# Optimization experiments

Measured on AMD Instinct MI355X. Metric: run time of the kernel, lower is better.

Reference implementation:

```python
import jax, jax.numpy as jnp
import numpy as np

N = 50000   # nodes
E = 500000  # edges
NEG_SLOPE = 0.2


def _edge_softmax(e, dst, n):
    # softmax over edges grouped by destination node (DGL edge_softmax)
    m = jax.ops.segment_max(e, dst, num_segments=n)          # [N,H]
    ex = jnp.exp(e - m[dst])
    s = jax.ops.segment_sum(ex, dst, num_segments=n)
    return ex / s[dst]


def _gat(h, W, al, ar, b, src, dst, heads, d, Wres=None, act=True):
    # DGL GATConv (eval mode, no dropout)
    n = h.shape[0]
    feat = (h @ W).reshape(n, heads, d)                      # [N,H,D]
    el = jnp.sum(feat * al[None], axis=-1)                   # [N,H]
    er = jnp.sum(feat * ar[None], axis=-1)                   # [N,H]
    e = jax.nn.leaky_relu(el[src] + er[dst], NEG_SLOPE)      # [E,H]
    a = _edge_softmax(e, dst, n)                             # [E,H]
    rst = jax.ops.segment_sum(feat[src] * a[..., None], dst, num_segments=n)  # [N,H,D]
    if Wres is not None:
        res = (h @ Wres).reshape(n, heads, d)
    else:
        res = h.reshape(n, heads, d)                         # identity residual (in == heads*d)
    rst = rst + res + b.reshape(1, heads, d)
    if act:
        rst = jax.nn.elu(rst)
    return rst.reshape(n, heads * d)


def _bn(x, g, b, m, v):
    # BatchNorm1d in eval mode
    return (x - m) * g * jax.lax.rsqrt(v + 1e-5) + b


def setup_inputs() -> dict:
    key = jax.random.key(0)
    ks = jax.random.split(key, 40)
    rn = lambda i, s: jax.random.normal(ks[i], s, jnp.float32) * 0.1
    inp = dict(
        node_feats=jax.random.normal(ks[0], (N, 128), jnp.float32),
        edge_feats=jax.random.normal(ks[1], (E, 64), jnp.float32),
        src=jax.random.randint(ks[2], (E,), 0, N, jnp.int32),
        dst=jax.random.randint(ks[3], (E,), 0, N, jnp.int32),
        # GAT layer 0: 128 -> 8 heads x 16
        W0=rn(4, (128, 128)), al0=rn(5, (8, 16)), ar0=rn(6, (8, 16)), b0=rn(7, (128,)),
        g0=1.0 + rn(8, (128,)), bt0=rn(9, (128,)), m0=rn(10, (128,)),
        v0=1.0 + 0.1 * jax.random.uniform(ks[11], (128,), jnp.float32),
        # GAT layer 1: 128 -> 8 heads x 8 (residual projection)
        W1=rn(12, (128, 64)), al1=rn(13, (8, 8)), ar1=rn(14, (8, 8)), b1=rn(15, (64,)),
        Wres1=rn(16, (128, 64)),
        g1=1.0 + rn(17, (64,)), bt1=rn(18, (64,)), m1=rn(19, (64,)),
        v1=1.0 + 0.1 * jax.random.uniform(ks[20], (64,), jnp.float32),
        # GAT layer 2: 64 -> 1 head x 32 (residual projection, no activation)
        W2=rn(21, (64, 32)), al2=rn(22, (1, 32)), ar2=rn(23, (1, 32)), b2=rn(24, (32,)),
        Wres2=rn(25, (64, 32)),
        g2=1.0 + rn(26, (32,)), bt2=rn(27, (32,)), m2=rn(28, (32,)),
        v2=1.0 + 0.1 * jax.random.uniform(ks[29], (32,), jnp.float32),
        # edge projection 64 -> 128
        We=rn(30, (64, 128)), be=rn(31, (128,)),
        # edge classifier: 192 -> 32 -> 16 -> 2
        Wc1=rn(32, (192, 32)), bc1=rn(33, (32,)),
        Wc2=rn(34, (32, 16)), bc2=rn(35, (16,)),
        Wc3=rn(36, (16, 2)), bc3=rn(37, (2,)),
    )
    return inp


def reference(node_feats, edge_feats, src, dst,
              W0, al0, ar0, b0, g0, bt0, m0, v0,
              W1, al1, ar1, b1, Wres1, g1, bt1, m1, v1,
              W2, al2, ar2, b2, Wres2, g2, bt2, m2, v2,
              We, be, Wc1, bc1, Wc2, bc2, Wc3, bc3):
    h = _bn(_gat(node_feats, W0, al0, ar0, b0, src, dst, 8, 16), g0, bt0, m0, v0)
    h = _bn(_gat(h, W1, al1, ar1, b1, src, dst, 8, 8, Wres1), g1, bt1, m1, v1)
    h = _bn(_gat(h, W2, al2, ar2, b2, src, dst, 1, 32, Wres2, act=False), g2, bt2, m2, v2)
    ef = jax.nn.relu(edge_feats @ We + be)                   # [E,128]
    rep = jnp.concatenate([h[src], h[dst], ef], axis=1)      # [E,192]
    z = jax.nn.relu(rep @ Wc1 + bc1)
    z = jax.nn.relu(z @ Wc2 + bc2)
    return z @ Wc3 + bc3                                     # [E,2]
```

## Files before the change

### kernel.cpp

```cpp
#include <hip/hip_runtime.h>
#include <cfloat>
#include <math.h>

#define NEG_SLOPE 0.2f

typedef short short8 __attribute__((ext_vector_type(8)));
typedef float f32x4 __attribute__((ext_vector_type(4)));

__device__ __forceinline__ short f2bf(float x) {
    unsigned u = __float_as_uint(x);
    u += 0x7fffu + ((u >> 16) & 1u);
    return (short)(u >> 16);
}

__device__ __forceinline__ void lds_fence() {
    __asm__ __volatile__("s_waitcnt lgkmcnt(0)" ::: "memory");
}


__global__ void count_deg_k(const int* __restrict__ dst, int* __restrict__ deg, int E) {
    int i = blockIdx.x * 256 + threadIdx.x;
    if (i < E) atomicAdd(&deg[dst[i]], 1);
}

__global__ void scan_k(const int* __restrict__ deg, int* __restrict__ off, int n) {
    __shared__ int part[1024];
    int tid = threadIdx.x;
    int chunk = (n + 1023) >> 10;
    int beg = tid * chunk;
    int end = min(beg + chunk, n);
    int s = 0;
    for (int i = beg; i < end; ++i) s += deg[i];
    part[tid] = s;
    __syncthreads();
    for (int d = 1; d < 1024; d <<= 1) {
        int v = (tid >= d) ? part[tid - d] : 0;
        __syncthreads();
        part[tid] += v;
        __syncthreads();
    }
    int run = (tid > 0) ? part[tid - 1] : 0;
    for (int i = beg; i < end; ++i) { off[i] = run; run += deg[i]; }
    if (tid == 1023) off[n] = part[1023];
}

__global__ void scatter_k(const int* __restrict__ src, const int* __restrict__ dst,
                          const int* __restrict__ off, int* __restrict__ cur,
                          int* __restrict__ srcp, int E) {
    int i = blockIdx.x * 256 + threadIdx.x;
    if (i >= E) return;
    int d = dst[i];
    int p = off[d] + atomicAdd(&cur[d], 1);
    srcp[p] = src[i];
}


__global__ void conv_w_k(const float* __restrict__ We, const float* __restrict__ Wc1p,
                         const float* __restrict__ Wc2,
                         short* __restrict__ WeTg, short* __restrict__ Wc1Tg,
                         short* __restrict__ Wc2Tg) {
    int t = blockIdx.x * 256 + threadIdx.x;
    if (t < 64 * 128) { int k = t >> 7, n = t & 127; WeTg[n * 64 + k] = f2bf(We[t]); }
    if (t < 128 * 32) { int k = t >> 5, n = t & 31; Wc1Tg[n * 128 + k] = f2bf(Wc1p[t]); }
    if (t < 32 * 16)  { int k = t >> 4, n = t & 15; Wc2Tg[n * 32 + k] = f2bf(Wc2[t]); }
}


template<int K, int OUT>
__global__ __launch_bounds__(256) void gemm2_k(const float* __restrict__ A,
                                               const float* __restrict__ B1, float* __restrict__ C1,
                                               const float* __restrict__ B2, float* __restrict__ C2,
                                               int nrows) {
    constexpr int CPT  = (OUT >= 64) ? 8 : 4;
    constexpr int CG   = OUT / CPT;
    constexpr int TY   = 256 / CG;
    constexpr int ROWS = TY * 4;
    constexpr int KT   = (K < 32) ? K : 32;
    constexpr int KTP  = KT + 4;

    __shared__ float As[ROWS * KTP];
    __shared__ float Bs[KT * OUT];

    const float* B = blockIdx.y ? B2 : B1;
    float*       C = blockIdx.y ? C2 : C1;

    int t = threadIdx.x;
    int tx = t % CG, ty = t / CG;
    int row0 = blockIdx.x * ROWS;

    float acc[4][CPT];
#pragma unroll
    for (int r = 0; r < 4; ++r)
#pragma unroll
        for (int c = 0; c < CPT; ++c) acc[r][c] = 0.f;

    for (int k0 = 0; k0 < K; k0 += KT) {
        __syncthreads();
#pragma unroll
        for (int i = t; i < ROWS * (KT / 4); i += 256) {
            int row = i / (KT / 4), c4 = i % (KT / 4);
            float4 v = {0.f, 0.f, 0.f, 0.f};
            if (row0 + row < nrows)
                v = *(const float4*)&A[(size_t)(row0 + row) * K + k0 + c4 * 4];
            *(float4*)&As[row * KTP + c4 * 4] = v;
        }
#pragma unroll
        for (int i = t; i < KT * (OUT / 4); i += 256) {
            int k = i / (OUT / 4), c4 = i % (OUT / 4);
            *(float4*)&Bs[k * OUT + c4 * 4] = *(const float4*)&B[(size_t)(k0 + k) * OUT + c4 * 4];
        }
        __syncthreads();

#pragma unroll
        for (int kk4 = 0; kk4 < KT / 4; ++kk4) {
            float4 a4[4];
#pragma unroll
            for (int r = 0; r < 4; ++r)
                a4[r] = *(const float4*)&As[(ty * 4 + r) * KTP + kk4 * 4];
#pragma unroll
            for (int j = 0; j < 4; ++j) {
                int kk = kk4 * 4 + j;
                float4 b4[CPT / 4];
#pragma unroll
                for (int c = 0; c < CPT / 4; ++c)
                    b4[c] = *(const float4*)&Bs[kk * OUT + tx * CPT + c * 4];
#pragma unroll
                for (int r = 0; r < 4; ++r) {
                    float a = ((const float*)&a4[r])[j];
#pragma unroll
                    for (int c = 0; c < CPT / 4; ++c) {
                        acc[r][c * 4 + 0] = fmaf(a, b4[c].x, acc[r][c * 4 + 0]);
                        acc[r][c * 4 + 1] = fmaf(a, b4[c].y, acc[r][c * 4 + 1]);
                        acc[r][c * 4 + 2] = fmaf(a, b4[c].z, acc[r][c * 4 + 2]);
                        acc[r][c * 4 + 3] = fmaf(a, b4[c].w, acc[r][c * 4 + 3]);
                    }
                }
            }
        }
    }

#pragma unroll
    for (int r = 0; r < 4; ++r) {
        int row = row0 + ty * 4 + r;
        if (row < nrows) {
#pragma unroll
            for (int c = 0; c < CPT / 4; ++c) {
                float4 v = {acc[r][c * 4 + 0], acc[r][c * 4 + 1], acc[r][c * 4 + 2], acc[r][c * 4 + 3]};
                *(float4*)&C[(size_t)row * OUT + tx * CPT + c * 4] = v;
            }
        }
    }
}


template<int H, int D>
__global__ void elr_k(const float* __restrict__ feat, const float* __restrict__ al,
                      const float* __restrict__ ar, float* __restrict__ el,
                      float* __restrict__ er, int n) {
    int i = blockIdx.x * 256 + threadIdx.x;
    if (i >= n * H) return;
    int h = i % H;
    const float* f = feat + (size_t)(i / H) * (H * D) + h * D;
    float sl = 0.f, sr = 0.f;
#pragma unroll
    for (int d = 0; d < D; ++d) {
        sl = fmaf(f[d], al[h * D + d], sl);
        sr = fmaf(f[d], ar[h * D + d], sr);
    }
    el[i] = sl; er[i] = sr;
}


template<int H, int D, bool ACT>
__global__ __launch_bounds__(256) void gat_node2_k(
    const int* __restrict__ off, const int* __restrict__ srcp,
    const float* __restrict__ el, const float* __restrict__ er,
    const float* __restrict__ feat,
    const float* __restrict__ res, const float* __restrict__ bias,
    const float* __restrict__ bg, const float* __restrict__ bb,
    const float* __restrict__ bm, const float* __restrict__ bv,
    float* __restrict__ hout, int N) {
    constexpr int HD = H * D;
    constexpr int CH = 64 / H;
    int wv_ = threadIdx.x >> 6;
    int lane = threadIdx.x & 63;
    int n = blockIdx.x * 4 + wv_;
    if (n >= N) return;
    int beg = off[n], end = off[n + 1];

    int hh = lane % H;
    int cc = lane / H;
    float ern = er[(size_t)n * H + hh];

    int k0 = lane;
    int h0 = k0 / D; if (h0 > H - 1) h0 = H - 1;
    int k1 = lane + 64, h1 = 0;
    if constexpr (HD > 64) h1 = k1 / D;

    float acc0 = 0.f, acc1 = 0.f, svp = 0.f;

    for (int i0 = beg; i0 < end; i0 += CH) {
        int iw = i0 + cc;
        float wv = 0.f;
        int sidx = 0;
        if (iw < end) {
            sidx = srcp[iw];
            float x = el[(size_t)sidx * H + hh] + ern;
            x = x > 0.f ? x : NEG_SLOPE * x;
            wv = __expf(x);
        }
        svp += wv;
        int lim = min(end - i0, CH);
        for (int r = 0; r < lim; ++r) {
            int sl = r * H;
            float w0 = __shfl(wv, sl + h0, 64);
            int s    = __shfl(sidx, sl + h0, 64);
            const float* frow = feat + (size_t)s * HD;
            if (HD > 64 || lane < HD)
                acc0 = fmaf(w0, frow[k0], acc0);
            if constexpr (HD > 64) {
                float w1 = __shfl(wv, sl + h1, 64);
                acc1 = fmaf(w1, frow[k1], acc1);
            }
        }
    }
#pragma unroll
    for (int mm = H; mm < 64; mm <<= 1) svp += __shfl_xor(svp, mm, 64);
    bool has_edges = end > beg;
    float inv0 = has_edges ? 1.f / __shfl(svp, h0, 64) : 0.f;
    float inv1 = 0.f;
    if constexpr (HD > 64) inv1 = has_edges ? 1.f / __shfl(svp, h1, 64) : 0.f;

#pragma unroll
    for (int r = 0; r < (HD + 63) / 64; ++r) {
        int k = lane + 64 * r;
        if (k < HD) {
            float a = (r == 0 ? acc0 * inv0 : acc1 * inv1);
            float x = a + res[(size_t)n * HD + k] + bias[k];
            if (ACT) x = x > 0.f ? x : expm1f(x);
            hout[(size_t)n * HD + k] = (x - bm[k]) * (bg[k] * rsqrtf(bv[k] + 1e-5f)) + bb[k];
        }
    }
}


__global__ __launch_bounds__(256) void edge_cls_k(
    const float* __restrict__ u1, const float* __restrict__ u2,
    const float* __restrict__ edf,
    const int* __restrict__ src, const int* __restrict__ dst,
    const short* __restrict__ WeTg, const float* __restrict__ be,
    const short* __restrict__ Wc1Tg, const float* __restrict__ bc1,
    const short* __restrict__ Wc2Tg, const float* __restrict__ bc2,
    const float* __restrict__ Wc3, const float* __restrict__ bc3,
    float* __restrict__ out, int E) {
    __shared__ short efA[4][16 * 136];
    __shared__ short z1A[4][16 * 40];
    __shared__ float z2A[4][16 * 20];

    int t = threadIdx.x;
    int w = t >> 6, lane = t & 63;
    int m = lane & 15, q = lane >> 4;
    short* efW = efA[w];
    short* z1W = z1A[w];
    float* z2W = z2A[w];

    int tiles = (E + 15) >> 4;
    int gw = blockIdx.x * 4 + w;
    int W  = gridDim.x * 4;

    float beh[8];
#pragma unroll
    for (int nt = 0; nt < 8; ++nt) beh[nt] = be[nt * 16 + m];
    float bc1h0 = bc1[m], bc1h1 = bc1[16 + m];
    float bc2h = bc2[m];
    float bc30 = bc3[0], bc31 = bc3[1];

    auto ldrow = [&](int tl, float4& a, float4& b, float4& c, float4& d) {
        int em = tl * 16 + m;
        const float* rp = edf + (size_t)(em < E ? em : E - 1) * 64;
        a = *(const float4*)(rp + q * 8);
        b = *(const float4*)(rp + q * 8 + 4);
        c = *(const float4*)(rp + 32 + q * 8);
        d = *(const float4*)(rp + 32 + q * 8 + 4);
    };

    int tile = gw;
    float4 p0 = {0,0,0,0}, p1 = p0, p2 = p0, p3 = p0;
    if (tile < tiles) ldrow(tile, p0, p1, p2, p3);

    for (; tile < tiles; tile += W) {
        float4 c0 = p0, c1 = p1, c2 = p2, c3 = p3;
        int tn = tile + W;
        if (tn < tiles) ldrow(tn, p0, p1, p2, p3);

        int e0w = tile * 16;

        float u1g[2][4], u2g[2][4];
#pragma unroll
        for (int r = 0; r < 4; ++r) {
            int e = e0w + q * 4 + r;
            int ec = e < E ? e : E - 1;
            int s = src[ec], d = dst[ec];
            u1g[0][r] = u1[(size_t)s * 32 + m];
            u1g[1][r] = u1[(size_t)s * 32 + 16 + m];
            u2g[0][r] = u2[(size_t)d * 32 + m];
            u2g[1][r] = u2[(size_t)d * 32 + 16 + m];
        }

        short8 A0, A1;
        A0[0] = f2bf(c0.x); A0[1] = f2bf(c0.y); A0[2] = f2bf(c0.z); A0[3] = f2bf(c0.w);
        A0[4] = f2bf(c1.x); A0[5] = f2bf(c1.y); A0[6] = f2bf(c1.z); A0[7] = f2bf(c1.w);
        A1[0] = f2bf(c2.x); A1[1] = f2bf(c2.y); A1[2] = f2bf(c2.z); A1[3] = f2bf(c2.w);
        A1[4] = f2bf(c3.x); A1[5] = f2bf(c3.y); A1[6] = f2bf(c3.z); A1[7] = f2bf(c3.w);

#pragma unroll
        for (int nt = 0; nt < 8; ++nt) {
            int col = nt * 16 + m;
            float bias = beh[nt];
            f32x4 acc = {bias, bias, bias, bias};
            short8 b0 = *(const short8*)&WeTg[col * 64 + q * 8];
            short8 b1 = *(const short8*)&WeTg[col * 64 + 32 + q * 8];
            acc = __builtin_amdgcn_mfma_f32_16x16x32_bf16(A0, b0, acc, 0, 0, 0);
            acc = __builtin_amdgcn_mfma_f32_16x16x32_bf16(A1, b1, acc, 0, 0, 0);
#pragma unroll
            for (int r = 0; r < 4; ++r)
                efW[(q * 4 + r) * 136 + col] = f2bf(fmaxf(acc[r], 0.f));
        }
        lds_fence();

        short8 Az[4];
#pragma unroll
        for (int kt = 0; kt < 4; ++kt)
            Az[kt] = *(const short8*)&efW[m * 136 + kt * 32 + q * 8];
#pragma unroll
        for (int nt = 0; nt < 2; ++nt) {
            int col = nt * 16 + m;
            float bias = nt ? bc1h1 : bc1h0;
            f32x4 acc = {bias, bias, bias, bias};
#pragma unroll
            for (int kt = 0; kt < 4; ++kt) {
                short8 b = *(const short8*)&Wc1Tg[col * 128 + kt * 32 + q * 8];
                acc = __builtin_amdgcn_mfma_f32_16x16x32_bf16(Az[kt], b, acc, 0, 0, 0);
            }
#pragma unroll
            for (int r = 0; r < 4; ++r) {
                float z = acc[r] + u1g[nt][r] + u2g[nt][r];
                z1W[(q * 4 + r) * 40 + col] = f2bf(fmaxf(z, 0.f));
            }
        }
        lds_fence();

        {
            short8 Az1 = *(const short8*)&z1W[m * 40 + q * 8];
            short8 Bz  = *(const short8*)&Wc2Tg[m * 32 + q * 8];
            f32x4 acc = {bc2h, bc2h, bc2h, bc2h};
            acc = __builtin_amdgcn_mfma_f32_16x16x32_bf16(Az1, Bz, acc, 0, 0, 0);
#pragma unroll
            for (int r = 0; r < 4; ++r)
                z2W[(q * 4 + r) * 20 + m] = fmaxf(acc[r], 0.f);
        }
        lds_fence();

        if (lane < 16) {
            int e = lane;
            int eg = e0w + e;
            if (eg < E) {
                float a0 = bc30, a1 = bc31;
#pragma unroll
                for (int k = 0; k < 16; ++k) {
                    float z = z2W[e * 20 + k];
                    a0 = fmaf(z, Wc3[k * 2], a0);
                    a1 = fmaf(z, Wc3[k * 2 + 1], a1);
                }
                float2 o = {a0, a1};
                *(float2*)&out[(size_t)eg * 2] = o;
            }
        }
        lds_fence();
    }
}


extern "C" void kernel_launch(void* const* d_in, const int* in_sizes, int n_in,
                              void* d_out, int out_size, void* d_ws, size_t ws_size,
                              hipStream_t stream) {
    const float* node_feats = (const float*)d_in[0];
    const float* edge_feats = (const float*)d_in[1];
    const int*   src  = (const int*)d_in[2];
    const int*   dst  = (const int*)d_in[3];
    const float* W0   = (const float*)d_in[4];
    const float* al0  = (const float*)d_in[5];
    const float* ar0  = (const float*)d_in[6];
    const float* b0   = (const float*)d_in[7];
    const float* g0   = (const float*)d_in[8];
    const float* bt0  = (const float*)d_in[9];
    const float* m0   = (const float*)d_in[10];
    const float* v0   = (const float*)d_in[11];
    const float* W1   = (const float*)d_in[12];
    const float* al1  = (const float*)d_in[13];
    const float* ar1  = (const float*)d_in[14];
    const float* b1   = (const float*)d_in[15];
    const float* Wr1  = (const float*)d_in[16];
    const float* g1   = (const float*)d_in[17];
    const float* bt1  = (const float*)d_in[18];
    const float* m1   = (const float*)d_in[19];
    const float* v1   = (const float*)d_in[20];
    const float* W2   = (const float*)d_in[21];
    const float* al2  = (const float*)d_in[22];
    const float* ar2  = (const float*)d_in[23];
    const float* b2   = (const float*)d_in[24];
    const float* Wr2  = (const float*)d_in[25];
    const float* g2   = (const float*)d_in[26];
    const float* bt2  = (const float*)d_in[27];
    const float* v2m  = (const float*)d_in[28];
    const float* v2v  = (const float*)d_in[29];
    const float* We   = (const float*)d_in[30];
    const float* be   = (const float*)d_in[31];
    const float* Wc1  = (const float*)d_in[32];
    const float* bc1  = (const float*)d_in[33];
    const float* Wc2  = (const float*)d_in[34];
    const float* bc2  = (const float*)d_in[35];
    const float* Wc3  = (const float*)d_in[36];
    const float* bc3  = (const float*)d_in[37];
    float* out = (float*)d_out;

    const int N = in_sizes[0] / 128;
    const int E = in_sizes[2];

    char* p = (char*)d_ws;
    auto alloc = [&](size_t bytes) -> void* {
        void* r = (void*)p;
        p += (bytes + 255) & ~(size_t)255;
        return r;
    };
    int*   deg  = (int*)alloc((size_t)N * 4);
    int*   cur  = (int*)alloc((size_t)N * 4);
    int*   off  = (int*)alloc((size_t)(N + 1) * 4);
    int*   srcp = (int*)alloc((size_t)E * 4);
    float* feat = (float*)alloc((size_t)N * 128 * 4);
    float* resf = (float*)alloc((size_t)N * 64 * 4);
    float* h1   = (float*)alloc((size_t)N * 128 * 4);
    float* h2   = (float*)alloc((size_t)N * 64 * 4);
    float* h3   = (float*)alloc((size_t)N * 32 * 4);
    float* el   = (float*)alloc((size_t)N * 8 * 4);
    float* er   = (float*)alloc((size_t)N * 8 * 4);
    short* WeTg = (short*)alloc((size_t)128 * 64 * 2);
    short* Wc1Tg= (short*)alloc((size_t)32 * 128 * 2);
    short* Wc2Tg= (short*)alloc((size_t)16 * 32 * 2);
    float* u1   = h1;
    float* u2   = h1 + (size_t)N * 32;

    hipMemsetAsync(deg, 0, (size_t)N * 4, stream);
    hipMemsetAsync(cur, 0, (size_t)N * 4, stream);

    int eb = (E + 255) / 256;
    count_deg_k<<<eb, 256, 0, stream>>>(dst, deg, E);
    scan_k<<<1, 1024, 0, stream>>>(deg, off, N);
    scatter_k<<<eb, 256, 0, stream>>>(src, dst, off, cur, srcp, E);
    conv_w_k<<<32, 256, 0, stream>>>(We, Wc1 + 64 * 32, Wc2, WeTg, Wc1Tg, Wc2Tg);

    int nb4 = (N + 3) / 4;

    gemm2_k<128,128><<<dim3((N + 63) / 64, 1), 256, 0, stream>>>(node_feats, W0, feat, W0, feat, N);
    elr_k<8,16><<<(N * 8 + 255) / 256, 256, 0, stream>>>(feat, al0, ar0, el, er, N);
    gat_node2_k<8,16,true><<<nb4, 256, 0, stream>>>(off, srcp, el, er, feat, node_feats,
                                                    b0, g0, bt0, m0, v0, h1, N);
    gemm2_k<128,64><<<dim3((N + 127) / 128, 2), 256, 0, stream>>>(h1, W1, feat, Wr1, resf, N);
    elr_k<8,8><<<(N * 8 + 255) / 256, 256, 0, stream>>>(feat, al1, ar1, el, er, N);
    gat_node2_k<8,8,true><<<nb4, 256, 0, stream>>>(off, srcp, el, er, feat, resf,
                                                   b1, g1, bt1, m1, v1, h2, N);
    gemm2_k<64,32><<<dim3((N + 127) / 128, 2), 256, 0, stream>>>(h2, W2, feat, Wr2, resf, N);
    elr_k<1,32><<<(N + 255) / 256, 256, 0, stream>>>(feat, al2, ar2, el, er, N);
    gat_node2_k<1,32,false><<<nb4, 256, 0, stream>>>(off, srcp, el, er, feat, resf,
                                                     b2, g2, bt2, v2m, v2v, h3, N);
    gemm2_k<32,32><<<dim3((N + 127) / 128, 2), 256, 0, stream>>>(h3, Wc1, u1, Wc1 + 32 * 32, u2, N);
    edge_cls_k<<<1024, 256, 0, stream>>>(u1, u2, edge_feats, src, dst,
                                         WeTg, be, Wc1Tg, bc1,
                                         Wc2Tg, bc2, Wc3, bc3, out, E);
}
```

Before: 680.0 us.

## Gather bf16 node features in GAT aggregation and prefetch edge-classifier gathers

The GEMM epilogue also writes a bf16 copy of the projected features, and the GAT aggregation kernels gather that copy instead of the fp32 rows. This halves the bytes moved by the random per-edge gathers. For the 128-wide layer, each lane now reads a packed pair of elements. The edge classifier also software-prefetches the next tile's u1/u2 gathers and stops hoisting bias values into registers. The cost is reduced precision in the aggregated features, plus an extra bf16 write per GEMM.

```diff
diff --git a/kernel.cpp b/kernel.cpp
--- a/kernel.cpp
+++ b/kernel.cpp
@@ -5,12 +5,16 @@
 #define NEG_SLOPE 0.2f
 
 typedef short short8 __attribute__((ext_vector_type(8)));
+typedef short short4v __attribute__((ext_vector_type(4)));
 typedef float f32x4 __attribute__((ext_vector_type(4)));
 
 __device__ __forceinline__ short f2bf(float x) {
     unsigned u = __float_as_uint(x);
     u += 0x7fffu + ((u >> 16) & 1u);
     return (short)(u >> 16);
+}
+__device__ __forceinline__ float bf2f(unsigned short s) {
+    return __uint_as_float((unsigned)s << 16);
 }
 
 __device__ __forceinline__ void lds_fence() {
@@ -66,11 +70,11 @@
 }
 
 
-template<int K, int OUT>
+template<int K, int OUT, bool B16>
 __global__ __launch_bounds__(256) void gemm2_k(const float* __restrict__ A,
                                                const float* __restrict__ B1, float* __restrict__ C1,
                                                const float* __restrict__ B2, float* __restrict__ C2,
-                                               int nrows) {
+                                               short* __restrict__ C1b, int nrows) {
     constexpr int CPT  = (OUT >= 64) ? 8 : 4;
     constexpr int CG   = OUT / CPT;
     constexpr int TY   = 256 / CG;
@@ -147,6 +151,19 @@
             for (int c = 0; c < CPT / 4; ++c) {
                 float4 v = {acc[r][c * 4 + 0], acc[r][c * 4 + 1], acc[r][c * 4 + 2], acc[r][c * 4 + 3]};
                 *(float4*)&C[(size_t)row * OUT + tx * CPT + c * 4] = v;
+            }
+            if (B16 && blockIdx.y == 0) {
+                if constexpr (CPT == 8) {
+                    short8 s;
+#pragma unroll
+                    for (int c = 0; c < 8; ++c) s[c] = f2bf(acc[r][c]);
+                    *(short8*)&C1b[(size_t)row * OUT + tx * CPT] = s;
+                } else {
+                    short4v s;
+#pragma unroll
+                    for (int c = 0; c < 4; ++c) s[c] = f2bf(acc[r][c]);
+                    *(short4v*)&C1b[(size_t)row * OUT + tx * CPT] = s;
+                }
             }
         }
     }
@@ -175,12 +192,13 @@
 __global__ __launch_bounds__(256) void gat_node2_k(
     const int* __restrict__ off, const int* __restrict__ srcp,
     const float* __restrict__ el, const float* __restrict__ er,
-    const float* __restrict__ feat,
+    const short* __restrict__ featb,
     const float* __restrict__ res, const float* __restrict__ bias,
     const float* __restrict__ bg, const float* __restrict__ bb,
     const float* __restrict__ bm, const float* __restrict__ bv,
     float* __restrict__ hout, int N) {
     constexpr int HD = H * D;
+    constexpr bool PAIR = (HD > 64);
     constexpr int CH = 64 / H;
     int wv_ = threadIdx.x >> 6;
     int lane = threadIdx.x & 63;
@@ -192,10 +210,8 @@
     int cc = lane / H;
     float ern = er[(size_t)n * H + hh];
 
-    int k0 = lane;
+    int k0 = PAIR ? 2 * lane : lane;
     int h0 = k0 / D; if (h0 > H - 1) h0 = H - 1;
-    int k1 = lane + 64, h1 = 0;
-    if constexpr (HD > 64) h1 = k1 / D;
 
     float acc0 = 0.f, acc1 = 0.f, svp = 0.f;
 
@@ -212,15 +228,16 @@
         svp += wv;
         int lim = min(end - i0, CH);
         for (int r = 0; r < lim; ++r) {
-            int sl = r * H;
-            float w0 = __shfl(wv, sl + h0, 64);
-            int s    = __shfl(sidx, sl + h0, 64);
-            const float* frow = feat + (size_t)s * HD;
-            if (HD > 64 || lane < HD)
-                acc0 = fmaf(w0, frow[k0], acc0);
-            if constexpr (HD > 64) {
-                float w1 = __shfl(wv, sl + h1, 64);
-                acc1 = fmaf(w1, frow[k1], acc1);
+            int sl = r * H + h0;
+            float w0 = __shfl(wv, sl, 64);
+            int s    = __shfl(sidx, sl, 64);
+            if constexpr (PAIR) {
+                ushort2 uv = *(const ushort2*)&featb[(size_t)s * HD + k0];
+                acc0 = fmaf(w0, bf2f(uv.x), acc0);
+                acc1 = fmaf(w0, bf2f(uv.y), acc1);
+            } else {
+                if (lane < HD)
+                    acc0 = fmaf(w0, bf2f((unsigned short)featb[(size_t)s * HD + k0]), acc0);
             }
         }
     }
@@ -228,15 +245,25 @@
     for (int mm = H; mm < 64; mm <<= 1) svp += __shfl_xor(svp, mm, 64);
     bool has_edges = end > beg;
     float inv0 = has_edges ? 1.f / __shfl(svp, h0, 64) : 0.f;
-    float inv1 = 0.f;
-    if constexpr (HD > 64) inv1 = has_edges ? 1.f / __shfl(svp, h1, 64) : 0.f;
-
-#pragma unroll
-    for (int r = 0; r < (HD + 63) / 64; ++r) {
-        int k = lane + 64 * r;
-        if (k < HD) {
-            float a = (r == 0 ? acc0 * inv0 : acc1 * inv1);
-            float x = a + res[(size_t)n * HD + k] + bias[k];
+
+    if constexpr (PAIR) {
+        float2 rs = *(const float2*)&res[(size_t)n * HD + k0];
+        float2 bi = *(const float2*)&bias[k0];
+        float2 gm = *(const float2*)&bm[k0];
+        float2 gv = *(const float2*)&bv[k0];
+        float2 gg = *(const float2*)&bg[k0];
+        float2 gb = *(const float2*)&bb[k0];
+        float x0 = acc0 * inv0 + rs.x + bi.x;
+        float x1 = acc1 * inv0 + rs.y + bi.y;
+        if (ACT) { x0 = x0 > 0.f ? x0 : expm1f(x0); x1 = x1 > 0.f ? x1 : expm1f(x1); }
+        float2 o;
+        o.x = (x0 - gm.x) * (gg.x * rsqrtf(gv.x + 1e-5f)) + gb.x;
+        o.y = (x1 - gm.y) * (gg.y * rsqrtf(gv.y + 1e-5f)) + gb.y;
+        *(float2*)&hout[(size_t)n * HD + k0] = o;
+    } else {
+        if (lane < HD) {
+            int k = k0;
+            float x = acc0 * inv0 + res[(size_t)n * HD + k] + bias[k];
             if (ACT) x = x > 0.f ? x : expm1f(x);
             hout[(size_t)n * HD + k] = (x - bm[k]) * (bg[k] * rsqrtf(bv[k] + 1e-5f)) + bb[k];
         }
@@ -268,10 +295,6 @@
     int gw = blockIdx.x * 4 + w;
     int W  = gridDim.x * 4;
 
-    float beh[8];
-#pragma unroll
-    for (int nt = 0; nt < 8; ++nt) beh[nt] = be[nt * 16 + m];
-    float bc1h0 = bc1[m], bc1h1 = bc1[16 + m];
     float bc2h = bc2[m];
     float bc30 = bc3[0], bc31 = bc3[1];
 
@@ -283,10 +306,23 @@
         c = *(const float4*)(rp + 32 + q * 8);
         d = *(const float4*)(rp + 32 + q * 8 + 4);
     };
+    auto ldu = [&](int tl, float (&ua)[2][4], float (&ub)[2][4]) {
+#pragma unroll
+        for (int r = 0; r < 4; ++r) {
+            int e = tl * 16 + q * 4 + r;
+            int ec = e < E ? e : E - 1;
+            int s = src[ec], d = dst[ec];
+            ua[0][r] = u1[(size_t)s * 32 + m];
+            ua[1][r] = u1[(size_t)s * 32 + 16 + m];
+            ub[0][r] = u2[(size_t)d * 32 + m];
+            ub[1][r] = u2[(size_t)d * 32 + 16 + m];
+        }
+    };
 
     int tile = gw;
     float4 p0 = {0,0,0,0}, p1 = p0, p2 = p0, p3 = p0;
-    if (tile < tiles) ldrow(tile, p0, p1, p2, p3);
+    float u1g[2][4], u2g[2][4];
+    if (tile < tiles) { ldrow(tile, p0, p1, p2, p3); ldu(tile, u1g, u2g); }
 
     for (; tile < tiles; tile += W) {
         float4 c0 = p0, c1 = p1, c2 = p2, c3 = p3;
@@ -294,18 +330,6 @@
         if (tn < tiles) ldrow(tn, p0, p1, p2, p3);
 
         int e0w = tile * 16;
-
-        float u1g[2][4], u2g[2][4];
-#pragma unroll
-        for (int r = 0; r < 4; ++r) {
-            int e = e0w + q * 4 + r;
-            int ec = e < E ? e : E - 1;
-            int s = src[ec], d = dst[ec];
-            u1g[0][r] = u1[(size_t)s * 32 + m];
-            u1g[1][r] = u1[(size_t)s * 32 + 16 + m];
-            u2g[0][r] = u2[(size_t)d * 32 + m];
-            u2g[1][r] = u2[(size_t)d * 32 + 16 + m];
-        }
 
         short8 A0, A1;
         A0[0] = f2bf(c0.x); A0[1] = f2bf(c0.y); A0[2] = f2bf(c0.z); A0[3] = f2bf(c0.w);
@@ -316,7 +340,7 @@
 #pragma unroll
         for (int nt = 0; nt < 8; ++nt) {
             int col = nt * 16 + m;
-            float bias = beh[nt];
+            float bias = be[col];
             f32x4 acc = {bias, bias, bias, bias};
             short8 b0 = *(const short8*)&WeTg[col * 64 + q * 8];
             short8 b1 = *(const short8*)&WeTg[col * 64 + 32 + q * 8];
@@ -335,7 +359,7 @@
 #pragma unroll
         for (int nt = 0; nt < 2; ++nt) {
             int col = nt * 16 + m;
-            float bias = nt ? bc1h1 : bc1h0;
+            float bias = bc1[col];
             f32x4 acc = {bias, bias, bias, bias};
 #pragma unroll
             for (int kt = 0; kt < 4; ++kt) {
@@ -349,6 +373,8 @@
             }
         }
         lds_fence();
+
+        if (tn < tiles) ldu(tn, u1g, u2g);
 
         {
             short8 Az1 = *(const short8*)&z1W[m * 40 + q * 8];
@@ -438,6 +464,7 @@
     int*   off  = (int*)alloc((size_t)(N + 1) * 4);
     int*   srcp = (int*)alloc((size_t)E * 4);
     float* feat = (float*)alloc((size_t)N * 128 * 4);
+    short* featb= (short*)alloc((size_t)N * 128 * 2);
     float* resf = (float*)alloc((size_t)N * 64 * 4);
     float* h1   = (float*)alloc((size_t)N * 128 * 4);
     float* h2   = (float*)alloc((size_t)N * 64 * 4);
@@ -461,19 +488,19 @@
 
     int nb4 = (N + 3) / 4;
 
-    gemm2_k<128,128><<<dim3((N + 63) / 64, 1), 256, 0, stream>>>(node_feats, W0, feat, W0, feat, N);
+    gemm2_k<128,128,true><<<dim3((N + 63) / 64, 1), 256, 0, stream>>>(node_feats, W0, feat, W0, resf, featb, N);
     elr_k<8,16><<<(N * 8 + 255) / 256, 256, 0, stream>>>(feat, al0, ar0, el, er, N);
-    gat_node2_k<8,16,true><<<nb4, 256, 0, stream>>>(off, srcp, el, er, feat, node_feats,
+    gat_node2_k<8,16,true><<<nb4, 256, 0, stream>>>(off, srcp, el, er, featb, node_feats,
                                                     b0, g0, bt0, m0, v0, h1, N);
-    gemm2_k<128,64><<<dim3((N + 127) / 128, 2), 256, 0, stream>>>(h1, W1, feat, Wr1, resf, N);
+    gemm2_k<128,64,true><<<dim3((N + 127) / 128, 2), 256, 0, stream>>>(h1, W1, feat, Wr1, resf, featb, N);
     elr_k<8,8><<<(N * 8 + 255) / 256, 256, 0, stream>>>(feat, al1, ar1, el, er, N);
-    gat_node2_k<8,8,true><<<nb4, 256, 0, stream>>>(off, srcp, el, er, feat, resf,
+    gat_node2_k<8,8,true><<<nb4, 256, 0, stream>>>(off, srcp, el, er, featb, resf,
                                                    b1, g1, bt1, m1, v1, h2, N);
-    gemm2_k<64,32><<<dim3((N + 127) / 128, 2), 256, 0, stream>>>(h2, W2, feat, Wr2, resf, N);
+    gemm2_k<64,32,true><<<dim3((N + 127) / 128, 2), 256, 0, stream>>>(h2, W2, feat, Wr2, resf, featb, N);
     elr_k<1,32><<<(N + 255) / 256, 256, 0, stream>>>(feat, al2, ar2, el, er, N);
-    gat_node2_k<1,32,false><<<nb4, 256, 0, stream>>>(off, srcp, el, er, feat, resf,
+    gat_node2_k<1,32,false><<<nb4, 256, 0, stream>>>(off, srcp, el, er, featb, resf,
                                                      b2, g2, bt2, v2m, v2v, h3, N);
-    gemm2_k<32,32><<<dim3((N + 127) / 128, 2), 256, 0, stream>>>(h3, Wc1, u1, Wc1 + 32 * 32, u2, N);
+    gemm2_k<32,32,false><<<dim3((N + 127) / 128, 2), 256, 0, stream>>>(h3, Wc1, u1, Wc1 + 32 * 32, u2, nullptr, N);
     edge_cls_k<<<1024, 256, 0, stream>>>(u1, u2, edge_feats, src, dst,
                                          WeTg, be, Wc1Tg, bc1,
                                          Wc2Tg, bc2, Wc3, bc3, out, E);
```

Result: no change. 669.7 us (-1.5%).
